# Kernel tuning notes

Hardware: AMD Instinct MI355X
Metric: run time of the kernel (lower is better)

Reference implementation:

```python
import jax, jax.numpy as jnp
import numpy as np

C = 512
GROUPS = 8
EPS = 1e-5


def setup_inputs() -> dict:
    key = jax.random.key(0)
    ks = jax.random.split(key, 7)
    b, c, h, w = 32, C, 32, 32
    x = jax.random.normal(ks[0], (b, c, h, w), dtype=jnp.float32)
    norm_gamma = jnp.ones((c,), dtype=jnp.float32)
    norm_beta = jnp.zeros((c,), dtype=jnp.float32)
    # 1x1 convs == per-pixel linear layers; store as [out, in] matrices
    qkv_w = jax.random.normal(ks[1], (3 * c, c), dtype=jnp.float32) * (1.0 / np.sqrt(c))
    qkv_b = jnp.zeros((3 * c,), dtype=jnp.float32)
    out_w = jax.random.normal(ks[2], (c, c), dtype=jnp.float32) * (1.0 / np.sqrt(c))
    out_b = jnp.zeros((c,), dtype=jnp.float32)
    return {"x": x, "norm_gamma": norm_gamma, "norm_beta": norm_beta,
            "qkv_w": qkv_w, "qkv_b": qkv_b, "out_w": out_w, "out_b": out_b}


def group_norm(x, gamma, beta):
    b, c, h, w = x.shape
    xg = x.reshape(b, GROUPS, c // GROUPS, h, w)
    mean = jnp.mean(xg, axis=(2, 3, 4), keepdims=True)
    var = jnp.var(xg, axis=(2, 3, 4), keepdims=True)
    xg = (xg - mean) * jax.lax.rsqrt(var + EPS)
    x = xg.reshape(b, c, h, w)
    return x * gamma[None, :, None, None] + beta[None, :, None, None]


def reference(x, norm_gamma, norm_beta, qkv_w, qkv_b, out_w, out_b):
    b, c, h, w = x.shape
    xn = group_norm(x, norm_gamma, norm_beta)
    # 1x1 conv: [b,c,h,w] -> [b,3c,h,w]
    qkv = jnp.einsum('oc,bchw->bohw', qkv_w, xn) + qkv_b[None, :, None, None]
    q, k, v = jnp.split(qkv.reshape(b, 3 * c, h * w), 3, axis=1)  # each [b,c,hw]
    scale = c ** (-0.5)
    attn = jnp.einsum('bci,bcj->bij', q, k) * scale  # [b, hw, hw]
    attn = jax.nn.softmax(attn, axis=-1)
    out = jnp.einsum('bij,bcj->bci', attn, v).reshape(b, c, h, w)
    out = jnp.einsum('oc,bchw->bohw', out_w, out) + out_b[None, :, None, None]
    return x + out
```

## Files before the change

kernel.cpp:

```cpp
#include <hip/hip_runtime.h>

#define HW 1024
#define CD 512

typedef __bf16 bf16x8 __attribute__((ext_vector_type(8)));
typedef float f32x4 __attribute__((ext_vector_type(4)));

__device__ __forceinline__ unsigned short f2bf(float f) {
    unsigned int u = __float_as_uint(f);
    u += 0x7fff + ((u >> 16) & 1);
    return (unsigned short)(u >> 16);
}
__device__ __forceinline__ float bf2f(unsigned short h) {
    return __uint_as_float((unsigned)h << 16);
}

#define AS1(p) ((__attribute__((address_space(1))) void*)(p))
#define AS3(p) ((__attribute__((address_space(3))) void*)(p))
#define GLD16(gp, lp) __builtin_amdgcn_global_load_lds(AS1(gp), AS3(lp), 16, 0, 0)

__global__ __launch_bounds__(256)
void gn_stats(const float* __restrict__ x, float* __restrict__ mean, float* __restrict__ rstd) {
    int bg = blockIdx.x;
    const float4* p4 = (const float4*)(x + (size_t)bg * 65536);
    int tid = threadIdx.x;
    float s = 0.f, ss = 0.f;
#pragma unroll 8
    for (int it = 0; it < 64; ++it) {
        float4 v = p4[tid + it * 256];
        s  += v.x + v.y + v.z + v.w;
        ss += v.x * v.x + v.y * v.y + v.z * v.z + v.w * v.w;
    }
#pragma unroll
    for (int d = 32; d > 0; d >>= 1) { s += __shfl_down(s, d); ss += __shfl_down(ss, d); }
    __shared__ float ls[4], lss[4];
    if ((tid & 63) == 0) { ls[tid >> 6] = s; lss[tid >> 6] = ss; }
    __syncthreads();
    if (tid == 0) {
        float S = ls[0] + ls[1] + ls[2] + ls[3];
        float SS = lss[0] + lss[1] + lss[2] + lss[3];
        float m = S * (1.f / 65536.f);
        float v = SS * (1.f / 65536.f) - m * m;
        mean[bg] = m;
        rstd[bg] = rsqrtf(v + 1e-5f);
    }
}

__global__ __launch_bounds__(256)
void gn_norm_t(const float* __restrict__ x, const float* __restrict__ mean, const float* __restrict__ rstd,
               const float* __restrict__ gamma, const float* __restrict__ beta,
               unsigned short* __restrict__ xnT) {
    __shared__ unsigned short tile[64][72];
    int i0 = blockIdx.x * 64, c0 = blockIdx.y * 64, b = blockIdx.z;
    float m = mean[b * 8 + blockIdx.y];
    float r = rstd[b * 8 + blockIdx.y];
    int tid = threadIdx.x;
    int tr = tid >> 4, tc = (tid & 15) * 4;
    const float* xb = x + ((size_t)b * CD + c0) * HW + i0;
#pragma unroll
    for (int p = 0; p < 4; ++p) {
        int c = tr + p * 16;
        float g = gamma[c0 + c] * r;
        float bb = beta[c0 + c] - m * g;
        float4 v = *(const float4*)(xb + (size_t)c * HW + tc);
        tile[c][tc + 0] = f2bf(v.x * g + bb);
        tile[c][tc + 1] = f2bf(v.y * g + bb);
        tile[c][tc + 2] = f2bf(v.z * g + bb);
        tile[c][tc + 3] = f2bf(v.w * g + bb);
    }
    __syncthreads();
    unsigned short* ob = xnT + ((size_t)b * HW + i0) * CD + c0;
#pragma unroll
    for (int p = 0; p < 4; ++p) {
        int ir = tr + p * 16;
        ushort4 u;
        u.x = tile[tc + 0][ir];
        u.y = tile[tc + 1][ir];
        u.z = tile[tc + 2][ir];
        u.w = tile[tc + 3][ir];
        *(ushort4*)(ob + (size_t)ir * CD + tc) = u;
    }
}

__global__ __launch_bounds__(256)
void tpose_bf16(const float* __restrict__ src, unsigned short* __restrict__ dst) {
    __shared__ unsigned short tile[64][72];
    int i0 = blockIdx.x * 64, c0 = blockIdx.y * 64;
    int tid = threadIdx.x;
    int tr = tid >> 4, tc = (tid & 15) * 4;
#pragma unroll
    for (int p = 0; p < 4; ++p) {
        int r = tr + p * 16;
        float4 v = *(const float4*)(src + (size_t)(i0 + r) * CD + c0 + tc);
        tile[r][tc + 0] = f2bf(v.x);
        tile[r][tc + 1] = f2bf(v.y);
        tile[r][tc + 2] = f2bf(v.z);
        tile[r][tc + 3] = f2bf(v.w);
    }
    __syncthreads();
#pragma unroll
    for (int p = 0; p < 4; ++p) {
        int ir = tr + p * 16;
        ushort4 u;
        u.x = tile[tc + 0][ir];
        u.y = tile[tc + 1][ir];
        u.z = tile[tc + 2][ir];
        u.w = tile[tc + 3][ir];
        *(ushort4*)(dst + (size_t)(c0 + ir) * CD + i0 + tc) = u;
    }
}

__global__ __launch_bounds__(256)
void cvt_bf16(const float* __restrict__ src, unsigned short* __restrict__ dst) {
    int i = blockIdx.x * 256 + threadIdx.x;
    float4 v = ((const float4*)src)[i];
    ushort4 u;
    u.x = f2bf(v.x); u.y = f2bf(v.y); u.z = f2bf(v.z); u.w = f2bf(v.w);
    ((ushort4*)dst)[i] = u;
}

__global__ __launch_bounds__(256)
void gvec_kernel(const float* __restrict__ wk, const float* __restrict__ bq,
                 float* __restrict__ g) {
    __shared__ float red[4][64];
    int d = blockIdx.x * 64 + (threadIdx.x & 63);
    int os = threadIdx.x >> 6;
    float acc = 0.f;
    for (int o = os * 128; o < os * 128 + 128; ++o)
        acc += wk[(size_t)o * CD + d] * bq[o];
    red[os][threadIdx.x & 63] = acc;
    __syncthreads();
    if (threadIdx.x < 64)
        g[blockIdx.x * 64 + threadIdx.x] = red[0][threadIdx.x] + red[1][threadIdx.x] +
                                           red[2][threadIdx.x] + red[3][threadIdx.x];
}

__global__ __launch_bounds__(256)
void bias2_kernel(const float* __restrict__ out_w, const float* __restrict__ bv,
                  float* __restrict__ bias2) {
    int wid = threadIdx.x >> 6, lane = threadIdx.x & 63;
    int o = blockIdx.x * 4 + wid;
    float acc = 0.f;
#pragma unroll
    for (int t = 0; t < 512; t += 64)
        acc += out_w[(size_t)o * CD + t + lane] * bv[t + lane];
#pragma unroll
    for (int d = 32; d > 0; d >>= 1) acc += __shfl_down(acc, d);
    if (lane == 0) bias2[o] = acc;
}

template<int EPI>
__global__ __launch_bounds__(256, 2)
void gemm_bt(const unsigned short* __restrict__ A, const unsigned short* __restrict__ B,
             void* __restrict__ Cv, const float* __restrict__ bias,
             const float* __restrict__ resid,
             int M, int N, int K, long long sA, long long sB, long long sC, long long sR) {
    unsigned nx = gridDim.x, ny = gridDim.y;
    unsigned lin = blockIdx.x + nx * (blockIdx.y + ny * blockIdx.z);
    unsigned nwg = nx * ny * gridDim.z;
    unsigned work = (lin & 7) * (nwg >> 3) + (lin >> 3);
    unsigned bx = work % nx; work /= nx;
    unsigned by = work % ny;
    unsigned bz = work / ny;

    A += (size_t)bz * sA;
    B += (size_t)bz * sB;
    int m0 = by * 128, n0 = bx * 128;

    __shared__ unsigned short lA[128 * 64];
    __shared__ unsigned short lB[128 * 64];

    int tid = threadIdx.x;
    int lane = tid & 63;
    int wr = (tid >> 6) >> 1, wc = (tid >> 6) & 1;

    f32x4 acc[4][4] = {};

    int strow[4], stcol[4];
#pragma unroll
    for (int s = 0; s < 4; ++s) {
        int row = (s * 256 + tid) >> 3;
        int g = (tid & 7) ^ (row & 7);
        strow[s] = row;
        stcol[s] = g * 8;
    }

    for (int k0 = 0; k0 < K; k0 += 64) {
#pragma unroll
        for (int s = 0; s < 4; ++s) {
            GLD16(A + (size_t)(m0 + strow[s]) * K + k0 + stcol[s], lA + (size_t)(s * 256 + tid) * 8);
            GLD16(B + (size_t)(n0 + strow[s]) * K + k0 + stcol[s], lB + (size_t)(s * 256 + tid) * 8);
        }
        __syncthreads();
#pragma unroll
        for (int kk = 0; kk < 64; kk += 32) {
            bf16x8 af[4], bfr[4];
#pragma unroll
            for (int m = 0; m < 4; ++m) {
                int row = wr * 64 + m * 16 + (lane & 15);
                int off = (row * 128 + (kk + (lane >> 4) * 8) * 2) ^ ((row & 7) << 4);
                af[m] = *(const bf16x8*)((const char*)lA + off);
            }
#pragma unroll
            for (int n = 0; n < 4; ++n) {
                int row = wc * 64 + n * 16 + (lane & 15);
                int off = (row * 128 + (kk + (lane >> 4) * 8) * 2) ^ ((row & 7) << 4);
                bfr[n] = *(const bf16x8*)((const char*)lB + off);
            }
#pragma unroll
            for (int m = 0; m < 4; ++m)
#pragma unroll
                for (int n = 0; n < 4; ++n)
                    acc[m][n] = __builtin_amdgcn_mfma_f32_16x16x32_bf16(af[m], bfr[n], acc[m][n], 0, 0, 0);
        }
        __syncthreads();
    }

    int rl = (lane >> 4) * 4;
    int cl = lane & 15;
    if (EPI == 2) {
        float* Cf = (float*)Cv + (size_t)bz * sC;
        const float* Rs = resid + (size_t)bz * sR;
#pragma unroll
        for (int m = 0; m < 4; ++m)
#pragma unroll
            for (int n = 0; n < 4; ++n) {
                int gm = m0 + wr * 64 + m * 16 + rl;
                int gn = n0 + wc * 64 + n * 16 + cl;
#pragma unroll
                for (int rg = 0; rg < 4; ++rg) {
                    size_t off = (size_t)(gm + rg) * N + gn;
                    Cf[off] = acc[m][n][rg] + bias[gm + rg] + Rs[off];
                }
            }
    } else {
        unsigned short* Cb = (unsigned short*)Cv + (size_t)bz * sC;
#pragma unroll
        for (int m = 0; m < 4; ++m)
#pragma unroll
            for (int n = 0; n < 4; ++n) {
                int gm = m0 + wr * 64 + m * 16 + rl;
                int gn = n0 + wc * 64 + n * 16 + cl;
#pragma unroll
                for (int rg = 0; rg < 4; ++rg) {
                    float v = acc[m][n][rg];
                    if (EPI == 0) v += bias[gn];
                    if (EPI == 1) v += bias[gm + rg];
                    Cb[(size_t)(gm + rg) * N + gn] = f2bf(v);
                }
            }
    }
}

__global__ __launch_bounds__(256, 2)
void scores_gemm(const unsigned short* __restrict__ T1, const unsigned short* __restrict__ xnT,
                 unsigned short* __restrict__ S, float* __restrict__ tmax, float* __restrict__ tsum) {
    unsigned nx = gridDim.x, ny = gridDim.y;
    unsigned lin = blockIdx.x + nx * (blockIdx.y + ny * blockIdx.z);
    unsigned nwg = nx * ny * gridDim.z;
    unsigned work = (lin & 7) * (nwg >> 3) + (lin >> 3);
    unsigned bx = work % nx; work /= nx;
    unsigned by = work % ny;
    unsigned bz = work / ny;

    const unsigned short* Ab = T1 + (size_t)bz * HW * CD;
    const unsigned short* Bb = xnT + (size_t)bz * HW * CD;
    int m0 = by * 128, n0 = bx * 128;

    __shared__ unsigned short lA[128 * 64];
    __shared__ unsigned short lB[128 * 64];
    __shared__ float redm[2][128];
    __shared__ float reds[2][128];

    int tid = threadIdx.x, lane = tid & 63;
    int wr = (tid >> 6) >> 1, wc = (tid >> 6) & 1;

    f32x4 acc[4][4] = {};
    int strow[4], stcol[4];
#pragma unroll
    for (int s = 0; s < 4; ++s) {
        int row = (s * 256 + tid) >> 3;
        int g = (tid & 7) ^ (row & 7);
        strow[s] = row;
        stcol[s] = g * 8;
    }

    for (int k0 = 0; k0 < CD; k0 += 64) {
#pragma unroll
        for (int s = 0; s < 4; ++s) {
            GLD16(Ab + (size_t)(m0 + strow[s]) * CD + k0 + stcol[s], lA + (size_t)(s * 256 + tid) * 8);
            GLD16(Bb + (size_t)(n0 + strow[s]) * CD + k0 + stcol[s], lB + (size_t)(s * 256 + tid) * 8);
        }
        __syncthreads();
#pragma unroll
        for (int kk = 0; kk < 64; kk += 32) {
            bf16x8 af[4], bfr[4];
#pragma unroll
            for (int m = 0; m < 4; ++m) {
                int row = wr * 64 + m * 16 + (lane & 15);
                int off = (row * 128 + (kk + (lane >> 4) * 8) * 2) ^ ((row & 7) << 4);
                af[m] = *(const bf16x8*)((const char*)lA + off);
            }
#pragma unroll
            for (int n = 0; n < 4; ++n) {
                int row = wc * 64 + n * 16 + (lane & 15);
                int off = (row * 128 + (kk + (lane >> 4) * 8) * 2) ^ ((row & 7) << 4);
                bfr[n] = *(const bf16x8*)((const char*)lB + off);
            }
#pragma unroll
            for (int m = 0; m < 4; ++m)
#pragma unroll
                for (int n = 0; n < 4; ++n)
                    acc[m][n] = __builtin_amdgcn_mfma_f32_16x16x32_bf16(af[m], bfr[n], acc[m][n], 0, 0, 0);
        }
        __syncthreads();
    }

    const float SL2E = 0.044194173824159216f * 1.4426950408889634f;
#pragma unroll
    for (int m = 0; m < 4; ++m)
#pragma unroll
        for (int n = 0; n < 4; ++n) acc[m][n] *= SL2E;

    int rl = (lane >> 4) * 4;
    int cl = lane & 15;

    float mr[4][4];
#pragma unroll
    for (int m = 0; m < 4; ++m)
#pragma unroll
        for (int rg = 0; rg < 4; ++rg)
            mr[m][rg] = fmaxf(fmaxf(acc[m][0][rg], acc[m][1][rg]),
                              fmaxf(acc[m][2][rg], acc[m][3][rg]));
#pragma unroll
    for (int d = 1; d < 16; d <<= 1)
#pragma unroll
        for (int m = 0; m < 4; ++m)
#pragma unroll
            for (int rg = 0; rg < 4; ++rg) mr[m][rg] = fmaxf(mr[m][rg], __shfl_xor(mr[m][rg], d));
    if ((lane & 15) == 0)
#pragma unroll
        for (int m = 0; m < 4; ++m)
#pragma unroll
            for (int rg = 0; rg < 4; ++rg) redm[wc][wr * 64 + m * 16 + rl + rg] = mr[m][rg];
    __syncthreads();
    float Mt[4][4];
#pragma unroll
    for (int m = 0; m < 4; ++m)
#pragma unroll
        for (int rg = 0; rg < 4; ++rg) {
            int row = wr * 64 + m * 16 + rl + rg;
            Mt[m][rg] = fmaxf(redm[0][row], redm[1][row]);
        }

    float sr[4][4] = {};
#pragma unroll
    for (int m = 0; m < 4; ++m)
#pragma unroll
        for (int n = 0; n < 4; ++n)
#pragma unroll
            for (int rg = 0; rg < 4; ++rg) sr[m][rg] += __builtin_amdgcn_exp2f(acc[m][n][rg] - Mt[m][rg]);
#pragma unroll
    for (int d = 1; d < 16; d <<= 1)
#pragma unroll
        for (int m = 0; m < 4; ++m)
#pragma unroll
            for (int rg = 0; rg < 4; ++rg) sr[m][rg] += __shfl_xor(sr[m][rg], d);
    if ((lane & 15) == 0)
#pragma unroll
        for (int m = 0; m < 4; ++m)
#pragma unroll
            for (int rg = 0; rg < 4; ++rg) reds[wc][wr * 64 + m * 16 + rl + rg] = sr[m][rg];
    __syncthreads();

    if (tid < 128) {
        float M = fmaxf(redm[0][tid], redm[1][tid]);
        float Z = reds[0][tid] + reds[1][tid];
        size_t o = ((size_t)bz * 8 + bx) * HW + m0 + tid;
        tmax[o] = M;
        tsum[o] = Z;
    }

    unsigned short* Sb = S + (size_t)bz * HW * HW;
#pragma unroll
    for (int m = 0; m < 4; ++m)
#pragma unroll
        for (int n = 0; n < 4; ++n) {
            int gm = m0 + wr * 64 + m * 16 + rl;
            int gn = n0 + wc * 64 + n * 16 + cl;
#pragma unroll
            for (int rg = 0; rg < 4; ++rg)
                Sb[(size_t)(gm + rg) * HW + gn] = f2bf(acc[m][n][rg]);
        }
}

__global__ __launch_bounds__(256)
void row_reduce(const float* __restrict__ tmax, const float* __restrict__ tsum,
                float* __restrict__ rowM, float* __restrict__ rowRZ) {
    int r = blockIdx.x * 256 + threadIdx.x;
    int b = r >> 10, i = r & 1023;
    const float* tm = tmax + (size_t)b * 8 * HW + i;
    const float* ts = tsum + (size_t)b * 8 * HW + i;
    float M = -1e30f;
#pragma unroll
    for (int jt = 0; jt < 8; ++jt) M = fmaxf(M, tm[(size_t)jt * HW]);
    float Z = 0.f;
#pragma unroll
    for (int jt = 0; jt < 8; ++jt) Z += ts[(size_t)jt * HW] * __builtin_amdgcn_exp2f(tm[(size_t)jt * HW] - M);
    rowM[r] = M;
    rowRZ[r] = 1.0f / Z;
}

__global__ __launch_bounds__(256)
void pnorm(unsigned short* __restrict__ SP, const float* __restrict__ rowM,
           const float* __restrict__ rowRZ) {
    size_t gid = (size_t)blockIdx.x * 256 + threadIdx.x;
    int row = (int)(gid >> 7);
    float M = rowM[row], rz = rowRZ[row];
    uint4 v = ((const uint4*)SP)[gid];
    unsigned* w = (unsigned*)&v;
#pragma unroll
    for (int k = 0; k < 4; ++k) {
        float a = bf2f((unsigned short)(w[k] & 0xffff));
        float c = bf2f((unsigned short)(w[k] >> 16));
        a = __builtin_amdgcn_exp2f(a - M) * rz;
        c = __builtin_amdgcn_exp2f(c - M) * rz;
        w[k] = (unsigned)f2bf(a) | ((unsigned)f2bf(c) << 16);
    }
    ((uint4*)SP)[gid] = v;
}

extern "C" void kernel_launch(void* const* d_in, const int* in_sizes, int n_in,
                              void* d_out, int out_size, void* d_ws, size_t ws_size,
                              hipStream_t stream) {
    const float* x      = (const float*)d_in[0];
    const float* gamma  = (const float*)d_in[1];
    const float* beta   = (const float*)d_in[2];
    const float* qkv_w  = (const float*)d_in[3];
    const float* qkv_b  = (const float*)d_in[4];
    const float* out_w  = (const float*)d_in[5];
    const float* out_b  = (const float*)d_in[6];

    char* ws = (char*)d_ws;
    unsigned short* xnT  = (unsigned short*)ws;
    unsigned short* vpr  = (unsigned short*)(ws + 33554432);
    unsigned short* SP   = (unsigned short*)(ws + 67108864);
    unsigned short* wqkT = (unsigned short*)(ws + 100663296);
    unsigned short* w2   = (unsigned short*)(ws + 101187584);
    float* gvec          = (float*)(ws + 101711872);
    float* bias2         = (float*)(ws + 101713920);
    float* meanp         = (float*)(ws + 101715968);
    float* rstdp         = (float*)(ws + 101716992);
    float* tmaxp         = (float*)(ws + 101718016);
    float* tsump         = (float*)(ws + 102766592);
    float* rowMp         = (float*)(ws + 103815168);
    float* rowRZp        = (float*)(ws + 103946240);

    unsigned short* wqT = SP;
    unsigned short* wkT = SP + 262144;
    unsigned short* wvT = SP + 524288;
    unsigned short* owb = SP + 786432;

    unsigned short* T1 = (unsigned short*)((char*)d_out + 33554432);
    float* outF = (float*)d_out;

    const float* wq_f = qkv_w;
    const float* wk_f = qkv_w + (size_t)512 * CD;
    const float* wv_f = qkv_w + (size_t)1024 * CD;

    gn_stats<<<256, 256, 0, stream>>>(x, meanp, rstdp);
    gn_norm_t<<<dim3(16, 8, 32), 256, 0, stream>>>(x, meanp, rstdp, gamma, beta, xnT);

    tpose_bf16<<<dim3(8, 8), 256, 0, stream>>>(wq_f, wqT);
    tpose_bf16<<<dim3(8, 8), 256, 0, stream>>>(wk_f, wkT);
    tpose_bf16<<<dim3(8, 8), 256, 0, stream>>>(wv_f, wvT);
    cvt_bf16<<<256, 256, 0, stream>>>(out_w, owb);
    gvec_kernel<<<8, 256, 0, stream>>>(wk_f, qkv_b, gvec);
    bias2_kernel<<<128, 256, 0, stream>>>(out_w, qkv_b + 1024, bias2);

    gemm_bt<3><<<dim3(4, 4, 1), 256, 0, stream>>>(wkT, wqT, wqkT, nullptr, nullptr,
        512, 512, 512, 0, 0, 0, 0);
    gemm_bt<3><<<dim3(4, 4, 1), 256, 0, stream>>>(owb, wvT, w2, nullptr, nullptr,
        512, 512, 512, 0, 0, 0, 0);

    gemm_bt<0><<<dim3(4, 8, 32), 256, 0, stream>>>(xnT, wqkT, T1, gvec, nullptr,
        1024, 512, 512, 1024LL * 512, 0, 1024LL * 512, 0);
    gemm_bt<1><<<dim3(8, 4, 32), 256, 0, stream>>>(w2, xnT, vpr, bias2, nullptr,
        512, 1024, 512, 0, 1024LL * 512, 512LL * 1024, 0);

    for (int h = 0; h < 2; ++h) {
        const unsigned short* T1h = T1 + (size_t)h * 16 * 1024 * 512;
        const unsigned short* xh  = xnT + (size_t)h * 16 * 1024 * 512;
        float* tmaxh  = tmaxp + (size_t)h * 16 * 8 * 1024;
        float* tsumh  = tsump + (size_t)h * 16 * 8 * 1024;
        float* rowMh  = rowMp + (size_t)h * 16 * 1024;
        float* rowRZh = rowRZp + (size_t)h * 16 * 1024;

        scores_gemm<<<dim3(8, 8, 16), 256, 0, stream>>>(T1h, xh, SP, tmaxh, tsumh);
        row_reduce<<<64, 256, 0, stream>>>(tmaxh, tsumh, rowMh, rowRZh);
        pnorm<<<8192, 256, 0, stream>>>(SP, rowMh, rowRZh);
        gemm_bt<2><<<dim3(8, 4, 16), 256, 0, stream>>>(
            vpr + (size_t)h * 16 * 512 * 1024, SP, outF + (size_t)h * 16 * 512 * 1024,
            out_b, x + (size_t)h * 16 * 512 * 1024,
            512, 1024, 1024, 512LL * 1024, 1024LL * 1024, 512LL * 1024, 512LL * 1024);
    }
    (void)in_sizes; (void)n_in; (void)out_size; (void)ws_size;
}
```

Measured before the change: 255.1 us.

## Double-buffer LDS staging and enlarge GEMM tiles to 256x128 with 512 threads

Both GEMM kernels now use 512-thread blocks with 256x128 output tiles and two LDS buffers, so global-to-LDS loads for the next K slice are issued while MFMAs run on the current one. This removes one barrier per K step and targets exposed load latency, and it also raises B-tile reuse. In exchange LDS per block doubles to about 96KB, allowing only one block per CU, and grids get smaller, so small GEMMs may leave CUs idle. Launch configurations and the scores-kernel reductions are resized to match.

```diff
diff --git a/kernel.cpp b/kernel.cpp
--- a/kernel.cpp
+++ b/kernel.cpp
@@ -150,7 +150,7 @@
 }
 
 template<int EPI>
-__global__ __launch_bounds__(256, 2)
+__global__ __launch_bounds__(512, 1)
 void gemm_bt(const unsigned short* __restrict__ A, const unsigned short* __restrict__ B,
              void* __restrict__ Cv, const float* __restrict__ bias,
              const float* __restrict__ resid,
@@ -165,47 +165,61 @@
 
     A += (size_t)bz * sA;
     B += (size_t)bz * sB;
-    int m0 = by * 128, n0 = bx * 128;
-
-    __shared__ unsigned short lA[128 * 64];
-    __shared__ unsigned short lB[128 * 64];
-
-    int tid = threadIdx.x;
-    int lane = tid & 63;
-    int wr = (tid >> 6) >> 1, wc = (tid >> 6) & 1;
+    int m0 = by * 256, n0 = bx * 128;
+
+    __shared__ unsigned short lA[2][256 * 64];
+    __shared__ unsigned short lB[2][128 * 64];
+
+    int tid = threadIdx.x, lane = tid & 63;
+    int wid = tid >> 6;
+    int wr = wid >> 1, wc = wid & 1;
 
     f32x4 acc[4][4] = {};
 
-    int strow[4], stcol[4];
+    int arow[4], acol[4], brow[2], bcol[2];
 #pragma unroll
     for (int s = 0; s < 4; ++s) {
-        int row = (s * 256 + tid) >> 3;
-        int g = (tid & 7) ^ (row & 7);
-        strow[s] = row;
-        stcol[s] = g * 8;
-    }
-
-    for (int k0 = 0; k0 < K; k0 += 64) {
-#pragma unroll
-        for (int s = 0; s < 4; ++s) {
-            GLD16(A + (size_t)(m0 + strow[s]) * K + k0 + stcol[s], lA + (size_t)(s * 256 + tid) * 8);
-            GLD16(B + (size_t)(n0 + strow[s]) * K + k0 + stcol[s], lB + (size_t)(s * 256 + tid) * 8);
-        }
-        __syncthreads();
+        int idx = s * 512 + tid;
+        arow[s] = idx >> 3;
+        acol[s] = ((idx & 7) ^ (arow[s] & 7)) * 8;
+    }
+#pragma unroll
+    for (int s = 0; s < 2; ++s) {
+        int idx = s * 512 + tid;
+        brow[s] = idx >> 3;
+        bcol[s] = ((idx & 7) ^ (brow[s] & 7)) * 8;
+    }
+
+    auto stage = [&](int buf, int k0) {
+#pragma unroll
+        for (int s = 0; s < 4; ++s)
+            GLD16(A + (size_t)(m0 + arow[s]) * K + k0 + acol[s], &lA[buf][(s * 512 + tid) * 8]);
+#pragma unroll
+        for (int s = 0; s < 2; ++s)
+            GLD16(B + (size_t)(n0 + brow[s]) * K + k0 + bcol[s], &lB[buf][(s * 512 + tid) * 8]);
+    };
+
+    int NT = K >> 6;
+    stage(0, 0);
+    __syncthreads();
+    int cur = 0;
+    for (int t = 0; t < NT; ++t) {
+        if (t + 1 < NT) stage(cur ^ 1, (t + 1) << 6);
+        const char* pa = (const char*)lA[cur];
+        const char* pb = (const char*)lB[cur];
 #pragma unroll
         for (int kk = 0; kk < 64; kk += 32) {
+            int koff = (kk + (lane >> 4) * 8) * 2;
             bf16x8 af[4], bfr[4];
 #pragma unroll
             for (int m = 0; m < 4; ++m) {
                 int row = wr * 64 + m * 16 + (lane & 15);
-                int off = (row * 128 + (kk + (lane >> 4) * 8) * 2) ^ ((row & 7) << 4);
-                af[m] = *(const bf16x8*)((const char*)lA + off);
+                af[m] = *(const bf16x8*)(pa + ((row * 128 + koff) ^ ((row & 7) << 4)));
             }
 #pragma unroll
             for (int n = 0; n < 4; ++n) {
                 int row = wc * 64 + n * 16 + (lane & 15);
-                int off = (row * 128 + (kk + (lane >> 4) * 8) * 2) ^ ((row & 7) << 4);
-                bfr[n] = *(const bf16x8*)((const char*)lB + off);
+                bfr[n] = *(const bf16x8*)(pb + ((row * 128 + koff) ^ ((row & 7) << 4)));
             }
 #pragma unroll
             for (int m = 0; m < 4; ++m)
@@ -214,6 +228,7 @@
                     acc[m][n] = __builtin_amdgcn_mfma_f32_16x16x32_bf16(af[m], bfr[n], acc[m][n], 0, 0, 0);
         }
         __syncthreads();
+        cur ^= 1;
     }
 
     int rl = (lane >> 4) * 4;
@@ -252,7 +267,7 @@
     }
 }
 
-__global__ __launch_bounds__(256, 2)
+__global__ __launch_bounds__(512, 1)
 void scores_gemm(const unsigned short* __restrict__ T1, const unsigned short* __restrict__ xnT,
                  unsigned short* __restrict__ S, float* __restrict__ tmax, float* __restrict__ tsum) {
     unsigned nx = gridDim.x, ny = gridDim.y;
@@ -265,47 +280,62 @@
 
     const unsigned short* Ab = T1 + (size_t)bz * HW * CD;
     const unsigned short* Bb = xnT + (size_t)bz * HW * CD;
-    int m0 = by * 128, n0 = bx * 128;
-
-    __shared__ unsigned short lA[128 * 64];
-    __shared__ unsigned short lB[128 * 64];
-    __shared__ float redm[2][128];
-    __shared__ float reds[2][128];
+    int m0 = by * 256, n0 = bx * 128;
+
+    __shared__ unsigned short lA[2][256 * 64];
+    __shared__ unsigned short lB[2][128 * 64];
+    __shared__ float redm[2][256];
+    __shared__ float reds[2][256];
 
     int tid = threadIdx.x, lane = tid & 63;
-    int wr = (tid >> 6) >> 1, wc = (tid >> 6) & 1;
+    int wid = tid >> 6;
+    int wr = wid >> 1, wc = wid & 1;
 
     f32x4 acc[4][4] = {};
-    int strow[4], stcol[4];
+
+    int arow[4], acol[4], brow[2], bcol[2];
 #pragma unroll
     for (int s = 0; s < 4; ++s) {
-        int row = (s * 256 + tid) >> 3;
-        int g = (tid & 7) ^ (row & 7);
-        strow[s] = row;
-        stcol[s] = g * 8;
-    }
-
-    for (int k0 = 0; k0 < CD; k0 += 64) {
-#pragma unroll
-        for (int s = 0; s < 4; ++s) {
-            GLD16(Ab + (size_t)(m0 + strow[s]) * CD + k0 + stcol[s], lA + (size_t)(s * 256 + tid) * 8);
-            GLD16(Bb + (size_t)(n0 + strow[s]) * CD + k0 + stcol[s], lB + (size_t)(s * 256 + tid) * 8);
-        }
-        __syncthreads();
+        int idx = s * 512 + tid;
+        arow[s] = idx >> 3;
+        acol[s] = ((idx & 7) ^ (arow[s] & 7)) * 8;
+    }
+#pragma unroll
+    for (int s = 0; s < 2; ++s) {
+        int idx = s * 512 + tid;
+        brow[s] = idx >> 3;
+        bcol[s] = ((idx & 7) ^ (brow[s] & 7)) * 8;
+    }
+
+    auto stage = [&](int buf, int k0) {
+#pragma unroll
+        for (int s = 0; s < 4; ++s)
+            GLD16(Ab + (size_t)(m0 + arow[s]) * CD + k0 + acol[s], &lA[buf][(s * 512 + tid) * 8]);
+#pragma unroll
+        for (int s = 0; s < 2; ++s)
+            GLD16(Bb + (size_t)(n0 + brow[s]) * CD + k0 + bcol[s], &lB[buf][(s * 512 + tid) * 8]);
+    };
+
+    stage(0, 0);
+    __syncthreads();
+    int cur = 0;
+    for (int t = 0; t < 8; ++t) {
+        if (t < 7) stage(cur ^ 1, (t + 1) << 6);
+        const char* pa = (const char*)lA[cur];
+        const char* pb = (const char*)lB[cur];
 #pragma unroll
         for (int kk = 0; kk < 64; kk += 32) {
+            int koff = (kk + (lane >> 4) * 8) * 2;
             bf16x8 af[4], bfr[4];
 #pragma unroll
             for (int m = 0; m < 4; ++m) {
                 int row = wr * 64 + m * 16 + (lane & 15);
-                int off = (row * 128 + (kk + (lane >> 4) * 8) * 2) ^ ((row & 7) << 4);
-                af[m] = *(const bf16x8*)((const char*)lA + off);
+                af[m] = *(const bf16x8*)(pa + ((row * 128 + koff) ^ ((row & 7) << 4)));
             }
 #pragma unroll
             for (int n = 0; n < 4; ++n) {
                 int row = wc * 64 + n * 16 + (lane & 15);
-                int off = (row * 128 + (kk + (lane >> 4) * 8) * 2) ^ ((row & 7) << 4);
-                bfr[n] = *(const bf16x8*)((const char*)lB + off);
+                bfr[n] = *(const bf16x8*)(pb + ((row * 128 + koff) ^ ((row & 7) << 4)));
             }
 #pragma unroll
             for (int m = 0; m < 4; ++m)
@@ -314,6 +344,7 @@
                     acc[m][n] = __builtin_amdgcn_mfma_f32_16x16x32_bf16(af[m], bfr[n], acc[m][n], 0, 0, 0);
         }
         __syncthreads();
+        cur ^= 1;
     }
 
     const float SL2E = 0.044194173824159216f * 1.4426950408889634f;
@@ -373,7 +404,7 @@
             for (int rg = 0; rg < 4; ++rg) reds[wc][wr * 64 + m * 16 + rl + rg] = sr[m][rg];
     __syncthreads();
 
-    if (tid < 128) {
+    if (tid < 256) {
         float M = fmaxf(redm[0][tid], redm[1][tid]);
         float Z = reds[0][tid] + reds[1][tid];
         size_t o = ((size_t)bz * 8 + bx) * HW + m0 + tid;
@@ -478,14 +509,14 @@
     gvec_kernel<<<8, 256, 0, stream>>>(wk_f, qkv_b, gvec);
     bias2_kernel<<<128, 256, 0, stream>>>(out_w, qkv_b + 1024, bias2);
 
-    gemm_bt<3><<<dim3(4, 4, 1), 256, 0, stream>>>(wkT, wqT, wqkT, nullptr, nullptr,
+    gemm_bt<3><<<dim3(4, 2, 1), 512, 0, stream>>>(wkT, wqT, wqkT, nullptr, nullptr,
         512, 512, 512, 0, 0, 0, 0);
-    gemm_bt<3><<<dim3(4, 4, 1), 256, 0, stream>>>(owb, wvT, w2, nullptr, nullptr,
+    gemm_bt<3><<<dim3(4, 2, 1), 512, 0, stream>>>(owb, wvT, w2, nullptr, nullptr,
         512, 512, 512, 0, 0, 0, 0);
 
-    gemm_bt<0><<<dim3(4, 8, 32), 256, 0, stream>>>(xnT, wqkT, T1, gvec, nullptr,
+    gemm_bt<0><<<dim3(4, 4, 32), 512, 0, stream>>>(xnT, wqkT, T1, gvec, nullptr,
         1024, 512, 512, 1024LL * 512, 0, 1024LL * 512, 0);
-    gemm_bt<1><<<dim3(8, 4, 32), 256, 0, stream>>>(w2, xnT, vpr, bias2, nullptr,
+    gemm_bt<1><<<dim3(8, 2, 32), 512, 0, stream>>>(w2, xnT, vpr, bias2, nullptr,
         512, 1024, 512, 0, 1024LL * 512, 512LL * 1024, 0);
 
     for (int h = 0; h < 2; ++h) {
@@ -496,10 +527,10 @@
         float* rowMh  = rowMp + (size_t)h * 16 * 1024;
         float* rowRZh = rowRZp + (size_t)h * 16 * 1024;
 
-        scores_gemm<<<dim3(8, 8, 16), 256, 0, stream>>>(T1h, xh, SP, tmaxh, tsumh);
+        scores_gemm<<<dim3(8, 4, 16), 512, 0, stream>>>(T1h, xh, SP, tmaxh, tsumh);
         row_reduce<<<64, 256, 0, stream>>>(tmaxh, tsumh, rowMh, rowRZh);
         pnorm<<<8192, 256, 0, stream>>>(SP, rowMh, rowRZh);
-        gemm_bt<2><<<dim3(8, 4, 16), 256, 0, stream>>>(
+        gemm_bt<2><<<dim3(8, 2, 16), 512, 0, stream>>>(
             vpr + (size_t)h * 16 * 512 * 1024, SP, outF + (size_t)h * 16 * 512 * 1024,
             out_b, x + (size_t)h * 16 * 512 * 1024,
             512, 1024, 1024, 512LL * 1024, 1024LL * 1024, 512LL * 1024, 512LL * 1024);
```

New measurement: 282.3 us. 10.6% more time.

## Fold softmax normalization into PV GEMM via per-tile rescale factors

Applied to the files above, without the earlier changes.

The scores kernel now stores exp2(s - tile max) as bf16 instead of raw scores. A small kernel computes one rescale factor per row per 128-column tile, exp(tile max - row max)/Z, and a new pv_gemm applies those factors to its partial accumulators every 128 k-columns. This removes the separate pnorm pass, which read and wrote the whole probability matrix. It adds a second accumulator set in pv_gemm, which raises register pressure. The three weight transposes are also merged into one launch.

```diff
diff --git a/kernel.cpp b/kernel.cpp
--- a/kernel.cpp
+++ b/kernel.cpp
@@ -83,8 +83,10 @@
 }
 
 __global__ __launch_bounds__(256)
-void tpose_bf16(const float* __restrict__ src, unsigned short* __restrict__ dst) {
+void tpose3_bf16(const float* __restrict__ qkv_w, unsigned short* __restrict__ dst0) {
     __shared__ unsigned short tile[64][72];
+    const float* src = qkv_w + (size_t)blockIdx.z * CD * CD;
+    unsigned short* dst = dst0 + (size_t)blockIdx.z * CD * CD;
     int i0 = blockIdx.x * 64, c0 = blockIdx.y * 64;
     int tid = threadIdx.x;
     int tr = tid >> 4, tc = (tid & 15) * 4;
@@ -153,8 +155,7 @@
 __global__ __launch_bounds__(256, 2)
 void gemm_bt(const unsigned short* __restrict__ A, const unsigned short* __restrict__ B,
              void* __restrict__ Cv, const float* __restrict__ bias,
-             const float* __restrict__ resid,
-             int M, int N, int K, long long sA, long long sB, long long sC, long long sR) {
+             int M, int N, int K, long long sA, long long sB, long long sC) {
     unsigned nx = gridDim.x, ny = gridDim.y;
     unsigned lin = blockIdx.x + nx * (blockIdx.y + ny * blockIdx.z);
     unsigned nwg = nx * ny * gridDim.z;
@@ -218,38 +219,21 @@
 
     int rl = (lane >> 4) * 4;
     int cl = lane & 15;
-    if (EPI == 2) {
-        float* Cf = (float*)Cv + (size_t)bz * sC;
-        const float* Rs = resid + (size_t)bz * sR;
-#pragma unroll
-        for (int m = 0; m < 4; ++m)
-#pragma unroll
-            for (int n = 0; n < 4; ++n) {
-                int gm = m0 + wr * 64 + m * 16 + rl;
-                int gn = n0 + wc * 64 + n * 16 + cl;
-#pragma unroll
-                for (int rg = 0; rg < 4; ++rg) {
-                    size_t off = (size_t)(gm + rg) * N + gn;
-                    Cf[off] = acc[m][n][rg] + bias[gm + rg] + Rs[off];
-                }
-            }
-    } else {
-        unsigned short* Cb = (unsigned short*)Cv + (size_t)bz * sC;
-#pragma unroll
-        for (int m = 0; m < 4; ++m)
-#pragma unroll
-            for (int n = 0; n < 4; ++n) {
-                int gm = m0 + wr * 64 + m * 16 + rl;
-                int gn = n0 + wc * 64 + n * 16 + cl;
-#pragma unroll
-                for (int rg = 0; rg < 4; ++rg) {
-                    float v = acc[m][n][rg];
-                    if (EPI == 0) v += bias[gn];
-                    if (EPI == 1) v += bias[gm + rg];
-                    Cb[(size_t)(gm + rg) * N + gn] = f2bf(v);
-                }
-            }
-    }
+    unsigned short* Cb = (unsigned short*)Cv + (size_t)bz * sC;
+#pragma unroll
+    for (int m = 0; m < 4; ++m)
+#pragma unroll
+        for (int n = 0; n < 4; ++n) {
+            int gm = m0 + wr * 64 + m * 16 + rl;
+            int gn = n0 + wc * 64 + n * 16 + cl;
+#pragma unroll
+            for (int rg = 0; rg < 4; ++rg) {
+                float v = acc[m][n][rg];
+                if (EPI == 0) v += bias[gn];
+                if (EPI == 1) v += bias[gm + rg];
+                Cb[(size_t)(gm + rg) * N + gn] = f2bf(v);
+            }
+        }
 }
 
 __global__ __launch_bounds__(256, 2)
@@ -359,7 +343,11 @@
 #pragma unroll
         for (int n = 0; n < 4; ++n)
 #pragma unroll
-            for (int rg = 0; rg < 4; ++rg) sr[m][rg] += __builtin_amdgcn_exp2f(acc[m][n][rg] - Mt[m][rg]);
+            for (int rg = 0; rg < 4; ++rg) {
+                float e = __builtin_amdgcn_exp2f(acc[m][n][rg] - Mt[m][rg]);
+                acc[m][n][rg] = e;
+                sr[m][rg] += e;
+            }
 #pragma unroll
     for (int d = 1; d < 16; d <<= 1)
 #pragma unroll
@@ -395,8 +383,8 @@
 }
 
 __global__ __launch_bounds__(256)
-void row_reduce(const float* __restrict__ tmax, const float* __restrict__ tsum,
-                float* __restrict__ rowM, float* __restrict__ rowRZ) {
+void rescale_kernel(const float* __restrict__ tmax, const float* __restrict__ tsum,
+                    float* __restrict__ rescale) {
     int r = blockIdx.x * 256 + threadIdx.x;
     int b = r >> 10, i = r & 1023;
     const float* tm = tmax + (size_t)b * 8 * HW + i;
@@ -407,27 +395,111 @@
     float Z = 0.f;
 #pragma unroll
     for (int jt = 0; jt < 8; ++jt) Z += ts[(size_t)jt * HW] * __builtin_amdgcn_exp2f(tm[(size_t)jt * HW] - M);
-    rowM[r] = M;
-    rowRZ[r] = 1.0f / Z;
-}
-
-__global__ __launch_bounds__(256)
-void pnorm(unsigned short* __restrict__ SP, const float* __restrict__ rowM,
-           const float* __restrict__ rowRZ) {
-    size_t gid = (size_t)blockIdx.x * 256 + threadIdx.x;
-    int row = (int)(gid >> 7);
-    float M = rowM[row], rz = rowRZ[row];
-    uint4 v = ((const uint4*)SP)[gid];
-    unsigned* w = (unsigned*)&v;
-#pragma unroll
-    for (int k = 0; k < 4; ++k) {
-        float a = bf2f((unsigned short)(w[k] & 0xffff));
-        float c = bf2f((unsigned short)(w[k] >> 16));
-        a = __builtin_amdgcn_exp2f(a - M) * rz;
-        c = __builtin_amdgcn_exp2f(c - M) * rz;
-        w[k] = (unsigned)f2bf(a) | ((unsigned)f2bf(c) << 16);
-    }
-    ((uint4*)SP)[gid] = v;
+    float rZ = 1.0f / Z;
+#pragma unroll
+    for (int jt = 0; jt < 8; ++jt)
+        rescale[((size_t)b * 8 + jt) * HW + i] = __builtin_amdgcn_exp2f(tm[(size_t)jt * HW] - M) * rZ;
+}
+
+__global__ __launch_bounds__(256, 2)
+void pv_gemm(const unsigned short* __restrict__ A, const unsigned short* __restrict__ B,
+             float* __restrict__ C, const float* __restrict__ bias,
+             const float* __restrict__ resid, const float* __restrict__ rescale) {
+    unsigned nx = gridDim.x, ny = gridDim.y;
+    unsigned lin = blockIdx.x + nx * (blockIdx.y + ny * blockIdx.z);
+    unsigned nwg = nx * ny * gridDim.z;
+    unsigned work = (lin & 7) * (nwg >> 3) + (lin >> 3);
+    unsigned bx = work % nx; work /= nx;
+    unsigned by = work % ny;
+    unsigned bz = work / ny;
+
+    A += (size_t)bz * 512 * 1024;
+    B += (size_t)bz * 1024 * 1024;
+    int m0 = by * 128, n0 = bx * 128;
+
+    __shared__ unsigned short lA[128 * 64];
+    __shared__ unsigned short lB[128 * 64];
+
+    int tid = threadIdx.x, lane = tid & 63;
+    int wr = (tid >> 6) >> 1, wc = (tid >> 6) & 1;
+    int cl = lane & 15;
+
+    f32x4 acc[4][4] = {};
+    f32x4 acct[4][4] = {};
+
+    float rs[8][4];
+#pragma unroll
+    for (int jt = 0; jt < 8; ++jt)
+#pragma unroll
+        for (int n = 0; n < 4; ++n)
+            rs[jt][n] = rescale[((size_t)bz * 8 + jt) * HW + n0 + wc * 64 + n * 16 + cl];
+
+    int strow[4], stcol[4];
+#pragma unroll
+    for (int s = 0; s < 4; ++s) {
+        int row = (s * 256 + tid) >> 3;
+        int g = (tid & 7) ^ (row & 7);
+        strow[s] = row;
+        stcol[s] = g * 8;
+    }
+
+#pragma unroll
+    for (int t = 0; t < 16; ++t) {
+        int k0 = t * 64;
+#pragma unroll
+        for (int s = 0; s < 4; ++s) {
+            GLD16(A + (size_t)(m0 + strow[s]) * 1024 + k0 + stcol[s], lA + (size_t)(s * 256 + tid) * 8);
+            GLD16(B + (size_t)(n0 + strow[s]) * 1024 + k0 + stcol[s], lB + (size_t)(s * 256 + tid) * 8);
+        }
+        __syncthreads();
+#pragma unroll
+        for (int kk = 0; kk < 64; kk += 32) {
+            bf16x8 af[4], bfr[4];
+#pragma unroll
+            for (int m = 0; m < 4; ++m) {
+                int row = wr * 64 + m * 16 + (lane & 15);
+                int off = (row * 128 + (kk + (lane >> 4) * 8) * 2) ^ ((row & 7) << 4);
+                af[m] = *(const bf16x8*)((const char*)lA + off);
+            }
+#pragma unroll
+            for (int n = 0; n < 4; ++n) {
+                int row = wc * 64 + n * 16 + (lane & 15);
+                int off = (row * 128 + (kk + (lane >> 4) * 8) * 2) ^ ((row & 7) << 4);
+                bfr[n] = *(const bf16x8*)((const char*)lB + off);
+            }
+#pragma unroll
+            for (int m = 0; m < 4; ++m)
+#pragma unroll
+                for (int n = 0; n < 4; ++n)
+                    acct[m][n] = __builtin_amdgcn_mfma_f32_16x16x32_bf16(af[m], bfr[n], acct[m][n], 0, 0, 0);
+        }
+        __syncthreads();
+        if (t & 1) {
+#pragma unroll
+            for (int m = 0; m < 4; ++m)
+#pragma unroll
+                for (int n = 0; n < 4; ++n) {
+                    acc[m][n] += acct[m][n] * rs[t >> 1][n];
+                    acct[m][n] = f32x4{0.f, 0.f, 0.f, 0.f};
+                }
+        }
+    }
+
+    int rl = (lane >> 4) * 4;
+    float* Cf = C + (size_t)bz * 512 * 1024;
+    const float* Rs = resid + (size_t)bz * 512 * 1024;
+#pragma unroll
+    for (int m = 0; m < 4; ++m)
+#pragma unroll
+        for (int n = 0; n < 4; ++n) {
+            int gm = m0 + wr * 64 + m * 16 + rl;
+            int gn = n0 + wc * 64 + n * 16 + cl;
+#pragma unroll
+            for (int rg = 0; rg < 4; ++rg) {
+                size_t off = (size_t)(gm + rg) * 1024 + gn;
+                Cf[off] = acc[m][n][rg] + bias[gm + rg] + Rs[off];
+            }
+        }
 }
 
 extern "C" void kernel_launch(void* const* d_in, const int* in_sizes, int n_in,
@@ -453,56 +525,48 @@
     float* rstdp         = (float*)(ws + 101716992);
     float* tmaxp         = (float*)(ws + 101718016);
     float* tsump         = (float*)(ws + 102766592);
-    float* rowMp         = (float*)(ws + 103815168);
-    float* rowRZp        = (float*)(ws + 103946240);
+    float* rescalep      = (float*)(ws + 103815168);
 
     unsigned short* wqT = SP;
-    unsigned short* wkT = SP + 262144;
     unsigned short* wvT = SP + 524288;
     unsigned short* owb = SP + 786432;
 
     unsigned short* T1 = (unsigned short*)((char*)d_out + 33554432);
     float* outF = (float*)d_out;
 
-    const float* wq_f = qkv_w;
     const float* wk_f = qkv_w + (size_t)512 * CD;
-    const float* wv_f = qkv_w + (size_t)1024 * CD;
 
     gn_stats<<<256, 256, 0, stream>>>(x, meanp, rstdp);
     gn_norm_t<<<dim3(16, 8, 32), 256, 0, stream>>>(x, meanp, rstdp, gamma, beta, xnT);
 
-    tpose_bf16<<<dim3(8, 8), 256, 0, stream>>>(wq_f, wqT);
-    tpose_bf16<<<dim3(8, 8), 256, 0, stream>>>(wk_f, wkT);
-    tpose_bf16<<<dim3(8, 8), 256, 0, stream>>>(wv_f, wvT);
+    tpose3_bf16<<<dim3(8, 8, 3), 256, 0, stream>>>(qkv_w, wqT);
     cvt_bf16<<<256, 256, 0, stream>>>(out_w, owb);
     gvec_kernel<<<8, 256, 0, stream>>>(wk_f, qkv_b, gvec);
     bias2_kernel<<<128, 256, 0, stream>>>(out_w, qkv_b + 1024, bias2);
 
-    gemm_bt<3><<<dim3(4, 4, 1), 256, 0, stream>>>(wkT, wqT, wqkT, nullptr, nullptr,
-        512, 512, 512, 0, 0, 0, 0);
-    gemm_bt<3><<<dim3(4, 4, 1), 256, 0, stream>>>(owb, wvT, w2, nullptr, nullptr,
-        512, 512, 512, 0, 0, 0, 0);
-
-    gemm_bt<0><<<dim3(4, 8, 32), 256, 0, stream>>>(xnT, wqkT, T1, gvec, nullptr,
-        1024, 512, 512, 1024LL * 512, 0, 1024LL * 512, 0);
-    gemm_bt<1><<<dim3(8, 4, 32), 256, 0, stream>>>(w2, xnT, vpr, bias2, nullptr,
-        512, 1024, 512, 0, 1024LL * 512, 512LL * 1024, 0);
+    unsigned short* wkT = wqT + 262144;
+    gemm_bt<3><<<dim3(4, 4, 1), 256, 0, stream>>>(wkT, wqT, wqkT, nullptr,
+        512, 512, 512, 0, 0, 0);
+    gemm_bt<3><<<dim3(4, 4, 1), 256, 0, stream>>>(owb, wvT, w2, nullptr,
+        512, 512, 512, 0, 0, 0);
+
+    gemm_bt<0><<<dim3(4, 8, 32), 256, 0, stream>>>(xnT, wqkT, T1, gvec,
+        1024, 512, 512, 1024LL * 512, 0, 1024LL * 512);
+    gemm_bt<1><<<dim3(8, 4, 32), 256, 0, stream>>>(w2, xnT, vpr, bias2,
+        512, 1024, 512, 0, 1024LL * 512, 512LL * 1024);
 
     for (int h = 0; h < 2; ++h) {
         const unsigned short* T1h = T1 + (size_t)h * 16 * 1024 * 512;
         const unsigned short* xh  = xnT + (size_t)h * 16 * 1024 * 512;
-        float* tmaxh  = tmaxp + (size_t)h * 16 * 8 * 1024;
-        float* tsumh  = tsump + (size_t)h * 16 * 8 * 1024;
-        float* rowMh  = rowMp + (size_t)h * 16 * 1024;
-        float* rowRZh = rowRZp + (size_t)h * 16 * 1024;
+        float* tmaxh = tmaxp + (size_t)h * 16 * 8 * 1024;
+        float* tsumh = tsump + (size_t)h * 16 * 8 * 1024;
 
         scores_gemm<<<dim3(8, 8, 16), 256, 0, stream>>>(T1h, xh, SP, tmaxh, tsumh);
-        row_reduce<<<64, 256, 0, stream>>>(tmaxh, tsumh, rowMh, rowRZh);
-        pnorm<<<8192, 256, 0, stream>>>(SP, rowMh, rowRZh);
-        gemm_bt<2><<<dim3(8, 4, 16), 256, 0, stream>>>(
-            vpr + (size_t)h * 16 * 512 * 1024, SP, outF + (size_t)h * 16 * 512 * 1024,
-            out_b, x + (size_t)h * 16 * 512 * 1024,
-            512, 1024, 1024, 512LL * 1024, 1024LL * 1024, 512LL * 1024, 512LL * 1024);
+        rescale_kernel<<<64, 256, 0, stream>>>(tmaxh, tsumh, rescalep);
+        pv_gemm<<<dim3(8, 4, 16), 256, 0, stream>>>(
+            vpr + (size_t)h * 16 * 512 * 1024, SP,
+            outF + (size_t)h * 16 * 512 * 1024, out_b,
+            x + (size_t)h * 16 * 512 * 1024, rescalep);
     }
     (void)in_sizes; (void)n_in; (void)out_size; (void)ws_size;
 }
```

Result: slower. 429.4 us (+68.3%).
